# Kernel optimization log

Measured on AMD Instinct MI355X. Metric: run time of the kernel, lower is better.

The kernel has to match this reference:

```python
import jax, jax.numpy as jnp
import numpy as np

B, H, S, D = 2, 16, 2048, 64

def setup_inputs() -> dict:
    key = jax.random.key(0)
    kq, kk, kv = jax.random.split(key, 3)
    query = jax.random.normal(kq, (B, H, S, D), dtype=jnp.float32)
    key_t = jax.random.normal(kk, (B, H, S, D), dtype=jnp.float32)
    value = jax.random.normal(kv, (B, H, S, D), dtype=jnp.float32)
    return {"query": query, "key": key_t, "value": value}

def reference(query, key, value):
    d_k = query.shape[-1]
    scale = 1.0 / jnp.sqrt(jnp.asarray(d_k, dtype=query.dtype))
    # scores: [B, H, S, S]
    scores = jnp.einsum('bhqd,bhkd->bhqk', query, key) * scale
    p_attn = jax.nn.softmax(scores, axis=-1)
    output = jnp.einsum('bhqk,bhkd->bhqd', p_attn, value)
    return (output, p_attn)
```

## Files before the change

kernel.cpp:

```cpp
#include <hip/hip_runtime.h>

#define SS 2048
#define DD 64
#define QB 64
#define KVB 64
#define NT (SS / KVB)

typedef unsigned short ushort_t;
typedef __attribute__((ext_vector_type(4)))  float f32x4;
typedef __attribute__((ext_vector_type(16))) float f32x16;
typedef __attribute__((ext_vector_type(8)))  short bf16x8;
typedef __attribute__((ext_vector_type(2)))  unsigned int u32x2;

static __device__ __forceinline__ unsigned short f2bf(float f) {
    unsigned u = __builtin_bit_cast(unsigned, f);
    u += 0x7FFFu + ((u >> 16) & 1u);
    return (unsigned short)(u >> 16);
}

static __device__ __forceinline__ f32x16 zero16() {
    f32x16 z;
#pragma unroll
    for (int i = 0; i < 16; ++i) z[i] = 0.f;
    return z;
}

union PFrag { bf16x8 v; unsigned w[4]; };

#define GLL16(src, dst) \
    __builtin_amdgcn_global_load_lds((const __attribute__((address_space(1))) void*)(src), \
                                     (__attribute__((address_space(3))) void*)(dst), 16, 0, 0)

__global__ void cvt_bf16(const float* __restrict__ src, ushort_t* __restrict__ dst,
                         int n8, float scale)
{
    int i = blockIdx.x * blockDim.x + threadIdx.x;
    if (i >= n8) return;
    f32x4 a = ((const f32x4*)src)[2 * i];
    f32x4 b = ((const f32x4*)src)[2 * i + 1];
    bf16x8 o;
#pragma unroll
    for (int j = 0; j < 4; ++j) o[j] = (short)f2bf(a[j] * scale);
#pragma unroll
    for (int j = 0; j < 4; ++j) o[4 + j] = (short)f2bf(b[j] * scale);
    ((bf16x8*)dst)[i] = o;
}

__global__ void transposeV(const float* __restrict__ V, ushort_t* __restrict__ Vt)
{
    __shared__ float tile[64][65];
    const int tid = threadIdx.x;
    const int hh = blockIdx.x >> 5;
    const int kt = blockIdx.x & 31;

#pragma unroll
    for (int it = 0; it < 4; ++it) {
        int m = it * 256 + tid;
        int r = m >> 4, c4 = m & 15;
        f32x4 v = *(const f32x4*)(V + ((size_t)(hh * SS + kt * 64 + r)) * DD + c4 * 4);
#pragma unroll
        for (int j = 0; j < 4; ++j) tile[r][c4 * 4 + j] = v[j];
    }
    __syncthreads();
#pragma unroll
    for (int it = 0; it < 2; ++it) {
        int m = it * 256 + tid;
        int d = m >> 3, c8 = m & 7;
        bf16x8 o;
#pragma unroll
        for (int j = 0; j < 8; ++j) o[j] = (short)f2bf(tile[c8 * 8 + j][d]);
        *(bf16x8*)(Vt + ((size_t)hh * DD + d) * SS + kt * 64 + c8 * 8) = o;
    }
}

__global__ __launch_bounds__(256, 4)
void attn_main4(const float* __restrict__ gQ, const ushort_t* __restrict__ Kbf,
                const ushort_t* __restrict__ Vtbf, float* __restrict__ gO,
                float* __restrict__ gP)
{
    __shared__ float lsm[4][32];
    __shared__ __attribute__((aligned(16))) char shraw[33792];
    ushort_t* stage = (ushort_t*)shraw;
    float*    osm   = (float*)shraw;

    const int tid  = threadIdx.x;
    const int lane = tid & 63;
    const int wave = tid >> 6;
    const int lo5  = lane & 31;
    const int hi   = lane >> 5;
    const int qs   = wave >> 1;
    const int sub  = wave & 1;

    const int bid  = blockIdx.x;
    const int wg   = (bid & 7) * 128 + (bid >> 3);
    const int head = wg >> 5;
    const int q0b  = (wg & 31) * QB;

    const float*    Qh = gQ   + (size_t)head * SS * DD;
    const ushort_t* Kh = Kbf  + (size_t)head * SS * DD;
    const ushort_t* Vh = Vtbf + (size_t)head * DD * SS;
    float* Oh = gO + (size_t)head * SS * DD;
    float* Ph = gP + (size_t)head * SS * SS;

    const float SCALE = 0.125f * 1.44269504088896340736f;

    const int qrow = q0b + qs * 32 + lo5;
    bf16x8 qf[4];
#pragma unroll
    for (int ks = 0; ks < 4; ++ks) {
        const float* qp = Qh + (size_t)qrow * DD + ks * 16 + hi * 8;
        f32x4 a = *(const f32x4*)(qp);
        f32x4 b = *(const f32x4*)(qp + 4);
        bf16x8 o;
#pragma unroll
        for (int j = 0; j < 4; ++j) o[j] = (short)f2bf(a[j] * SCALE);
#pragma unroll
        for (int j = 0; j < 4; ++j) o[4 + j] = (short)f2bf(b[j] * SCALE);
        qf[ks] = o;
    }

    const int lgrp = lane >> 3;
    const int lchk = (lane & 7) ^ lgrp;
    const ushort_t* srcK[2]; const ushort_t* srcV[2];
#pragma unroll
    for (int j = 0; j < 2; ++j) {
        int W = wave * 2 + j;
        srcK[j] = Kh + (size_t)(W * 8 + lgrp) * DD + lchk * 8;
        srcV[j] = Vh + (size_t)(W * 8 + lgrp) * SS + lchk * 8;
    }
    const int kvl = sub * 32 + lo5;

#pragma unroll
    for (int j = 0; j < 2; ++j) GLL16(srcK[j], stage + (wave * 2 + j) * 512);
    __syncthreads();

    float ls0 = 0.f, ls1 = 0.f;
    for (int t = 0; t < NT; ++t) {
        const int buf = t & 1;
        if (t + 1 < NT) {
#pragma unroll
            for (int j = 0; j < 2; ++j)
                GLL16(srcK[j] + (size_t)(t + 1) * KVB * DD,
                      stage + (buf ^ 1) * 8192 + (wave * 2 + j) * 512);
        }
        const ushort_t* Ksb = stage + buf * 8192;
        f32x16 acc = zero16();
#pragma unroll
        for (int ks = 0; ks < 4; ++ks) {
            bf16x8 kf = *(const bf16x8*)(Ksb + kvl * 64 + ((((ks * 2) + hi) ^ (kvl & 7)) << 3));
            acc = __builtin_amdgcn_mfma_f32_32x32x16_bf16(kf, qf[ks], acc, 0, 0, 0);
        }
#pragma unroll
        for (int r = 0; r < 16; r += 2) {
            ls0 += __builtin_exp2f(acc[r]);
            ls1 += __builtin_exp2f(acc[r + 1]);
        }
        __syncthreads();
    }
    float lsum = ls0 + ls1;
    lsum += __shfl_xor(lsum, 32);
    lsm[wave][lo5] = lsum;
    __syncthreads();
    const float rinv = 1.0f / (lsm[qs * 2][lo5] + lsm[qs * 2 + 1][lo5]);

    f32x16 o0 = zero16(), o1 = zero16();
    float* prow_base = Ph + (size_t)qrow * SS;

#pragma unroll
    for (int j = 0; j < 2; ++j) {
        GLL16(srcK[j], stage + (wave * 2 + j) * 512);
        GLL16(srcV[j], stage + 4096 + (wave * 2 + j) * 512);
    }
    __syncthreads();

    for (int t = 0; t < NT; ++t) {
        const int buf = t & 1;
        if (t + 1 < NT) {
#pragma unroll
            for (int j = 0; j < 2; ++j) {
                GLL16(srcK[j] + (size_t)(t + 1) * KVB * DD,
                      stage + (buf ^ 1) * 8192 + (wave * 2 + j) * 512);
                GLL16(srcV[j] + (size_t)(t + 1) * KVB,
                      stage + (buf ^ 1) * 8192 + 4096 + (wave * 2 + j) * 512);
            }
        }
        const ushort_t* Ksb = stage + buf * 8192;
        const ushort_t* Vtb = Ksb + 4096;

        f32x16 acc = zero16();
#pragma unroll
        for (int ks = 0; ks < 4; ++ks) {
            bf16x8 kf = *(const bf16x8*)(Ksb + kvl * 64 + ((((ks * 2) + hi) ^ (kvl & 7)) << 3));
            acc = __builtin_amdgcn_mfma_f32_32x32x16_bf16(kf, qf[ks], acc, 0, 0, 0);
        }
        float pr[16];
#pragma unroll
        for (int r = 0; r < 16; ++r) pr[r] = __builtin_exp2f(acc[r]);

        float* prow = prow_base + t * KVB + sub * 32;
#pragma unroll
        for (int g = 0; g < 4; ++g) {
            f32x4 st = { pr[4*g+0] * rinv, pr[4*g+1] * rinv, pr[4*g+2] * rinv, pr[4*g+3] * rinv };
            *(f32x4*)(prow + g * 8 + hi * 4) = st;
        }

        unsigned u[8];
#pragma unroll
        for (int j = 0; j < 8; ++j)
            u[j] = (unsigned)f2bf(pr[2*j]) | ((unsigned)f2bf(pr[2*j+1]) << 16);

        unsigned s0 = __shfl_xor(u[0], 32), s1 = __shfl_xor(u[1], 32);
        unsigned s2 = __shfl_xor(u[2], 32), s3 = __shfl_xor(u[3], 32);
        unsigned s4 = __shfl_xor(u[4], 32), s5 = __shfl_xor(u[5], 32);
        unsigned s6 = __shfl_xor(u[6], 32), s7 = __shfl_xor(u[7], 32);
        PFrag pf0, pf1;
        pf0.w[0] = hi ? s2 : u[0];  pf0.w[1] = hi ? s3 : u[1];
        pf0.w[2] = hi ? u[2] : s0;  pf0.w[3] = hi ? u[3] : s1;
        pf1.w[0] = hi ? s6 : u[4];  pf1.w[1] = hi ? s7 : u[5];
        pf1.w[2] = hi ? u[6] : s4;  pf1.w[3] = hi ? u[7] : s5;

#pragma unroll
        for (int dt = 0; dt < 2; ++dt) {
            int drow = dt * 32 + lo5;
            int c0 = ((sub * 4) + 0 + hi) ^ (drow & 7);
            int c1 = ((sub * 4) + 2 + hi) ^ (drow & 7);
            bf16x8 vf0 = *(const bf16x8*)(Vtb + drow * 64 + (c0 << 3));
            bf16x8 vf1 = *(const bf16x8*)(Vtb + drow * 64 + (c1 << 3));
            f32x16& od = dt ? o1 : o0;
            od = __builtin_amdgcn_mfma_f32_32x32x16_bf16(vf0, pf0.v, od, 0, 0, 0);
            od = __builtin_amdgcn_mfma_f32_32x32x16_bf16(vf1, pf1.v, od, 0, 0, 0);
        }

        __syncthreads();
    }

#pragma unroll
    for (int dt = 0; dt < 2; ++dt) {
        const f32x16& od = dt ? o1 : o0;
#pragma unroll
        for (int g = 0; g < 4; ++g) {
#pragma unroll
            for (int j = 0; j < 4; ++j) {
                int d = dt * 32 + g * 8 + hi * 4 + j;
                osm[(wave * 64 + d) * 33 + lo5] = od[4 * g + j];
            }
        }
    }
    __syncthreads();
    {
        const int p  = tid >> 7;
        const int q  = (tid >> 2) & 31;
        const int d0 = (tid & 3) * 16;
        const float rq = 1.0f / (lsm[2 * p][q] + lsm[2 * p + 1][q]);
        float* op = Oh + (size_t)(q0b + p * 32 + q) * DD + d0;
#pragma unroll
        for (int v4 = 0; v4 < 4; ++v4) {
            f32x4 st;
#pragma unroll
            for (int j = 0; j < 4; ++j) {
                int d = d0 + v4 * 4 + j;
                st[j] = (osm[((2 * p) * 64 + d) * 33 + q] +
                         osm[((2 * p + 1) * 64 + d) * 33 + q]) * rq;
            }
            *(f32x4*)(op + v4 * 4) = st;
        }
    }
}

__global__ __launch_bounds__(256, 2)
void attn_fused(const float* __restrict__ gQ, const float* __restrict__ gK,
                const float* __restrict__ gV, float* __restrict__ gO,
                float* __restrict__ gP)
{
    __shared__ unsigned short Qs[128 * DD];
    __shared__ unsigned short Ks[64 * DD];
    __shared__ unsigned short Vt[DD * 64];

    const int tid  = threadIdx.x;
    const int lane = tid & 63;
    const int wave = tid >> 6;
    const int lo5  = lane & 31;
    const int hi   = lane >> 5;

    const int head = blockIdx.x >> 4;
    const int q0b  = (blockIdx.x & 15) * 128;

    const float* Qh = gQ + (size_t)head * SS * DD;
    const float* Kh = gK + (size_t)head * SS * DD;
    const float* Vh = gV + (size_t)head * SS * DD;
    float* Oh = gO + (size_t)head * SS * DD;
    float* Ph = gP + (size_t)head * SS * SS;

    const float SCALE = 0.125f * 1.44269504088896340736f;

#pragma unroll
    for (int it = 0; it < 8; ++it) {
        int m = it * 256 + tid;
        int q = m >> 4, d4 = m & 15;
        f32x4 v = *(const f32x4*)(Qh + (size_t)(q0b + q) * DD + d4 * 4);
        unsigned a = (unsigned)f2bf(v.x * SCALE) | ((unsigned)f2bf(v.y * SCALE) << 16);
        unsigned b = (unsigned)f2bf(v.z * SCALE) | ((unsigned)f2bf(v.w * SCALE) << 16);
        u32x2 w; w.x = a; w.y = b;
        *(u32x2*)(Qs + q * 64 + d4 * 4) = w;
    }
    __syncthreads();

    const int qrow = wave * 32 + lo5;
    bf16x8 qf[4];
#pragma unroll
    for (int ks = 0; ks < 4; ++ks)
        qf[ks] = *(const bf16x8*)(Qs + qrow * 64 + ks * 16 + hi * 8);

    auto stageK = [&](int kv0) {
#pragma unroll
        for (int it = 0; it < 4; ++it) {
            int m = it * 256 + tid;
            int kv = m >> 4, d4 = m & 15;
            f32x4 v = *(const f32x4*)(Kh + (size_t)(kv0 + kv) * DD + d4 * 4);
            unsigned a = (unsigned)f2bf(v.x) | ((unsigned)f2bf(v.y) << 16);
            unsigned b = (unsigned)f2bf(v.z) | ((unsigned)f2bf(v.w) << 16);
            int c16 = (d4 >> 1) ^ (kv & 7);
            u32x2 w; w.x = a; w.y = b;
            *(u32x2*)(Ks + kv * 64 + c16 * 8 + (d4 & 1) * 4) = w;
        }
    };
    auto stageV = [&](int kv0) {
#pragma unroll
        for (int it = 0; it < 2; ++it) {
            int m = it * 256 + tid;
            int kv2 = m >> 4, d4 = m & 15;
            const float* p0 = Vh + (size_t)(kv0 + kv2 * 2) * DD + d4 * 4;
            f32x4 v0 = *(const f32x4*)(p0);
            f32x4 v1 = *(const f32x4*)(p0 + DD);
#pragma unroll
            for (int c = 0; c < 4; ++c) {
                int d = d4 * 4 + c;
                unsigned u = (unsigned)f2bf(v0[c]) | ((unsigned)f2bf(v1[c]) << 16);
                int c16 = (kv2 >> 2) ^ (d & 7);
                *(unsigned*)(Vt + d * 64 + c16 * 8 + (kv2 & 3) * 2) = u;
            }
        }
    };

    float m_run = -1e30f, l_run = 0.f;
    for (int kv0 = 0; kv0 < SS; kv0 += 64) {
        __syncthreads();
        stageK(kv0);
        __syncthreads();
#pragma unroll
        for (int sub = 0; sub < 2; ++sub) {
            f32x16 acc = zero16();
            int kvl = sub * 32 + lo5;
#pragma unroll
            for (int ks = 0; ks < 4; ++ks) {
                bf16x8 kf = *(const bf16x8*)(Ks + kvl * 64 + ((((ks * 2) + hi) ^ (kvl & 7)) << 3));
                acc = __builtin_amdgcn_mfma_f32_32x32x16_bf16(kf, qf[ks], acc, 0, 0, 0);
            }
            float tm = acc[0];
#pragma unroll
            for (int r = 1; r < 16; ++r) tm = fmaxf(tm, acc[r]);
            float mn = fmaxf(m_run, tm);
            float sum = 0.f;
#pragma unroll
            for (int r = 0; r < 16; ++r) sum += __builtin_exp2f(acc[r] - mn);
            l_run = l_run * __builtin_exp2f(m_run - mn) + sum;
            m_run = mn;
        }
    }
    {
        float mo = __shfl_xor(m_run, 32);
        float mf = fmaxf(m_run, mo);
        float la = l_run * __builtin_exp2f(m_run - mf);
        float lb = __shfl_xor(la, 32);
        l_run = la + lb;
        m_run = mf;
    }
    const float rinv = 1.0f / l_run;

    f32x16 o0 = zero16(), o1 = zero16();
    const int qg = q0b + wave * 32 + lo5;
    float* prow_base = Ph + (size_t)qg * SS;

    for (int kv0 = 0; kv0 < SS; kv0 += 64) {
        __syncthreads();
        stageK(kv0);
        stageV(kv0);
        __syncthreads();
#pragma unroll
        for (int sub = 0; sub < 2; ++sub) {
            f32x16 acc = zero16();
            int kvl = sub * 32 + lo5;
#pragma unroll
            for (int ks = 0; ks < 4; ++ks) {
                bf16x8 kf = *(const bf16x8*)(Ks + kvl * 64 + ((((ks * 2) + hi) ^ (kvl & 7)) << 3));
                acc = __builtin_amdgcn_mfma_f32_32x32x16_bf16(kf, qf[ks], acc, 0, 0, 0);
            }
            float pr[16];
#pragma unroll
            for (int r = 0; r < 16; ++r) pr[r] = __builtin_exp2f(acc[r] - m_run);

            float* prow = prow_base + kv0 + sub * 32;
#pragma unroll
            for (int g = 0; g < 4; ++g) {
                f32x4 st = { pr[4*g+0] * rinv, pr[4*g+1] * rinv, pr[4*g+2] * rinv, pr[4*g+3] * rinv };
                *(f32x4*)(prow + g * 8 + hi * 4) = st;
            }

            unsigned u[8];
#pragma unroll
            for (int j = 0; j < 8; ++j)
                u[j] = (unsigned)f2bf(pr[2*j]) | ((unsigned)f2bf(pr[2*j+1]) << 16);

            unsigned s0 = __shfl_xor(u[0], 32), s1 = __shfl_xor(u[1], 32);
            unsigned s2 = __shfl_xor(u[2], 32), s3 = __shfl_xor(u[3], 32);
            unsigned s4 = __shfl_xor(u[4], 32), s5 = __shfl_xor(u[5], 32);
            unsigned s6 = __shfl_xor(u[6], 32), s7 = __shfl_xor(u[7], 32);
            PFrag pf0, pf1;
            pf0.w[0] = hi ? s2 : u[0];  pf0.w[1] = hi ? s3 : u[1];
            pf0.w[2] = hi ? u[2] : s0;  pf0.w[3] = hi ? u[3] : s1;
            pf1.w[0] = hi ? s6 : u[4];  pf1.w[1] = hi ? s7 : u[5];
            pf1.w[2] = hi ? u[6] : s4;  pf1.w[3] = hi ? u[7] : s5;

#pragma unroll
            for (int dt = 0; dt < 2; ++dt) {
                int drow = dt * 32 + lo5;
                int c0 = ((sub * 4) + 0 + hi) ^ (drow & 7);
                int c1 = ((sub * 4) + 2 + hi) ^ (drow & 7);
                bf16x8 vf0 = *(const bf16x8*)(Vt + drow * 64 + (c0 << 3));
                bf16x8 vf1 = *(const bf16x8*)(Vt + drow * 64 + (c1 << 3));
                f32x16& od = dt ? o1 : o0;
                od = __builtin_amdgcn_mfma_f32_32x32x16_bf16(vf0, pf0.v, od, 0, 0, 0);
                od = __builtin_amdgcn_mfma_f32_32x32x16_bf16(vf1, pf1.v, od, 0, 0, 0);
            }
        }
    }

    float* orow = Oh + (size_t)qg * DD;
#pragma unroll
    for (int dt = 0; dt < 2; ++dt) {
        const f32x16& od = dt ? o1 : o0;
#pragma unroll
        for (int g = 0; g < 4; ++g) {
            f32x4 st = { od[4*g+0] * rinv, od[4*g+1] * rinv, od[4*g+2] * rinv, od[4*g+3] * rinv };
            *(f32x4*)(orow + dt * 32 + g * 8 + hi * 4) = st;
        }
    }
}

extern "C" void kernel_launch(void* const* d_in, const int* in_sizes, int n_in,
                              void* d_out, int out_size, void* d_ws, size_t ws_size,
                              hipStream_t stream) {
    const float* Q = (const float*)d_in[0];
    const float* K = (const float*)d_in[1];
    const float* V = (const float*)d_in[2];
    float* O = (float*)d_out;
    float* P = O + (size_t)2 * 16 * SS * DD;

    const size_t HD = (size_t)32 * SS * DD;
    const size_t need = 2 * HD * sizeof(ushort_t);

    if (ws_size >= need) {
        ushort_t* Kbf  = (ushort_t*)d_ws;
        ushort_t* Vtbf = Kbf + HD;
        int n8 = (int)(HD / 8);
        hipLaunchKernelGGL(cvt_bf16, dim3(n8 / 256), dim3(256), 0, stream, K, Kbf, n8, 1.0f);
        hipLaunchKernelGGL(transposeV, dim3(1024), dim3(256), 0, stream, V, Vtbf);
        hipLaunchKernelGGL(attn_main4, dim3(1024), dim3(256), 0, stream, Q, Kbf, Vtbf, O, P);
    } else {
        hipLaunchKernelGGL(attn_fused, dim3(512), dim3(256), 0, stream, Q, K, V, O, P);
    }
}
```

Before: 212.3 us.

## Process two Q tiles per block, fusing second tile's row-sum pass into first's output pass

Each workgroup now handles 128 query rows as two 64-row halves. The row-sum pass for the second half is folded into the P/O pass of the first half, sharing the K tile loads and fragments, so the blocks make three sweeps over K/V instead of four. The K bf16 conversion and the V transpose are merged into a single prep launch to save one kernel launch. In exchange the grid is halved to 512 blocks with launch bounds of 2, and LDS and register use go up, which lowers occupancy.

```diff
diff --git a/kernel.cpp b/kernel.cpp
--- a/kernel.cpp
+++ b/kernel.cpp
@@ -2,7 +2,7 @@
 
 #define SS 2048
 #define DD 64
-#define QB 64
+#define QB 128
 #define KVB 64
 #define NT (SS / KVB)
 
@@ -31,28 +31,26 @@
     __builtin_amdgcn_global_load_lds((const __attribute__((address_space(1))) void*)(src), \
                                      (__attribute__((address_space(3))) void*)(dst), 16, 0, 0)
 
-__global__ void cvt_bf16(const float* __restrict__ src, ushort_t* __restrict__ dst,
-                         int n8, float scale)
+__global__ void prep(const float* __restrict__ K, const float* __restrict__ V,
+                     ushort_t* __restrict__ Kbf, ushort_t* __restrict__ Vt)
 {
-    int i = blockIdx.x * blockDim.x + threadIdx.x;
-    if (i >= n8) return;
-    f32x4 a = ((const f32x4*)src)[2 * i];
-    f32x4 b = ((const f32x4*)src)[2 * i + 1];
-    bf16x8 o;
-#pragma unroll
-    for (int j = 0; j < 4; ++j) o[j] = (short)f2bf(a[j] * scale);
-#pragma unroll
-    for (int j = 0; j < 4; ++j) o[4 + j] = (short)f2bf(b[j] * scale);
-    ((bf16x8*)dst)[i] = o;
-}
-
-__global__ void transposeV(const float* __restrict__ V, ushort_t* __restrict__ Vt)
-{
+    const int tid = threadIdx.x;
+    if (blockIdx.x < 2048) {
+        int i = blockIdx.x * 256 + tid;
+        f32x4 a = ((const f32x4*)K)[2 * i];
+        f32x4 b = ((const f32x4*)K)[2 * i + 1];
+        bf16x8 o;
+#pragma unroll
+        for (int j = 0; j < 4; ++j) o[j] = (short)f2bf(a[j]);
+#pragma unroll
+        for (int j = 0; j < 4; ++j) o[4 + j] = (short)f2bf(b[j]);
+        ((bf16x8*)Kbf)[i] = o;
+        return;
+    }
     __shared__ float tile[64][65];
-    const int tid = threadIdx.x;
-    const int hh = blockIdx.x >> 5;
-    const int kt = blockIdx.x & 31;
-
+    const int bid2 = blockIdx.x - 2048;
+    const int hh = bid2 >> 5;
+    const int kt = bid2 & 31;
 #pragma unroll
     for (int it = 0; it < 4; ++it) {
         int m = it * 256 + tid;
@@ -73,15 +71,14 @@
     }
 }
 
-__global__ __launch_bounds__(256, 4)
-void attn_main4(const float* __restrict__ gQ, const ushort_t* __restrict__ Kbf,
-                const ushort_t* __restrict__ Vtbf, float* __restrict__ gO,
-                float* __restrict__ gP)
+__global__ __launch_bounds__(256, 2)
+void attn_main11(const float* __restrict__ gQ, const ushort_t* __restrict__ Kbf,
+                 const ushort_t* __restrict__ Vtbf, float* __restrict__ gO,
+                 float* __restrict__ gP)
 {
-    __shared__ float lsm[4][32];
-    __shared__ __attribute__((aligned(16))) char shraw[33792];
-    ushort_t* stage = (ushort_t*)shraw;
-    float*    osm   = (float*)shraw;
+    __shared__ float lsm[2][4][32];
+    __shared__ __attribute__((aligned(16))) ushort_t stage[2][8192];
+    __shared__ float osm[4 * 64 * 33];
 
     const int tid  = threadIdx.x;
     const int lane = tid & 63;
@@ -92,9 +89,9 @@
     const int sub  = wave & 1;
 
     const int bid  = blockIdx.x;
-    const int wg   = (bid & 7) * 128 + (bid >> 3);
-    const int head = wg >> 5;
-    const int q0b  = (wg & 31) * QB;
+    const int wg   = (bid & 7) * 64 + (bid >> 3);
+    const int head = wg >> 4;
+    const int q0b  = (wg & 15) * QB;
 
     const float*    Qh = gQ   + (size_t)head * SS * DD;
     const ushort_t* Kh = Kbf  + (size_t)head * SS * DD;
@@ -104,20 +101,21 @@
 
     const float SCALE = 0.125f * 1.44269504088896340736f;
 
-    const int qrow = q0b + qs * 32 + lo5;
-    bf16x8 qf[4];
-#pragma unroll
-    for (int ks = 0; ks < 4; ++ks) {
-        const float* qp = Qh + (size_t)qrow * DD + ks * 16 + hi * 8;
-        f32x4 a = *(const f32x4*)(qp);
-        f32x4 b = *(const f32x4*)(qp + 4);
-        bf16x8 o;
-#pragma unroll
-        for (int j = 0; j < 4; ++j) o[j] = (short)f2bf(a[j] * SCALE);
-#pragma unroll
-        for (int j = 0; j < 4; ++j) o[4 + j] = (short)f2bf(b[j] * SCALE);
-        qf[ks] = o;
-    }
+    bf16x8 qfh[2][4];
+#pragma unroll
+    for (int h = 0; h < 2; ++h)
+#pragma unroll
+        for (int ks = 0; ks < 4; ++ks) {
+            const float* qp = Qh + (size_t)(q0b + h * 64 + qs * 32 + lo5) * DD + ks * 16 + hi * 8;
+            f32x4 a = *(const f32x4*)(qp);
+            f32x4 b = *(const f32x4*)(qp + 4);
+            bf16x8 o;
+#pragma unroll
+            for (int j = 0; j < 4; ++j) o[j] = (short)f2bf(a[j] * SCALE);
+#pragma unroll
+            for (int j = 0; j < 4; ++j) o[4 + j] = (short)f2bf(b[j] * SCALE);
+            qfh[h][ks] = o;
+        }
 
     const int lgrp = lane >> 3;
     const int lchk = (lane & 7) ^ lgrp;
@@ -131,7 +129,7 @@
     const int kvl = sub * 32 + lo5;
 
 #pragma unroll
-    for (int j = 0; j < 2; ++j) GLL16(srcK[j], stage + (wave * 2 + j) * 512);
+    for (int j = 0; j < 2; ++j) GLL16(srcK[j], &stage[0][(wave * 2 + j) * 512]);
     __syncthreads();
 
     float ls0 = 0.f, ls1 = 0.f;
@@ -140,15 +138,14 @@
         if (t + 1 < NT) {
 #pragma unroll
             for (int j = 0; j < 2; ++j)
-                GLL16(srcK[j] + (size_t)(t + 1) * KVB * DD,
-                      stage + (buf ^ 1) * 8192 + (wave * 2 + j) * 512);
-        }
-        const ushort_t* Ksb = stage + buf * 8192;
+                GLL16(srcK[j] + (size_t)(t + 1) * KVB * DD, &stage[buf ^ 1][(wave * 2 + j) * 512]);
+        }
+        const ushort_t* Ksb = &stage[buf][0];
         f32x16 acc = zero16();
 #pragma unroll
         for (int ks = 0; ks < 4; ++ks) {
             bf16x8 kf = *(const bf16x8*)(Ksb + kvl * 64 + ((((ks * 2) + hi) ^ (kvl & 7)) << 3));
-            acc = __builtin_amdgcn_mfma_f32_32x32x16_bf16(kf, qf[ks], acc, 0, 0, 0);
+            acc = __builtin_amdgcn_mfma_f32_32x32x16_bf16(kf, qfh[0][ks], acc, 0, 0, 0);
         }
 #pragma unroll
         for (int r = 0; r < 16; r += 2) {
@@ -157,81 +154,100 @@
         }
         __syncthreads();
     }
-    float lsum = ls0 + ls1;
-    lsum += __shfl_xor(lsum, 32);
-    lsm[wave][lo5] = lsum;
-    __syncthreads();
-    const float rinv = 1.0f / (lsm[qs * 2][lo5] + lsm[qs * 2 + 1][lo5]);
+    {
+        float l = ls0 + ls1;
+        l += __shfl_xor(l, 32);
+        lsm[0][wave][lo5] = l;
+    }
+    __syncthreads();
+    const float rinv0 = 1.0f / (lsm[0][qs * 2][lo5] + lsm[0][qs * 2 + 1][lo5]);
 
     f32x16 o0 = zero16(), o1 = zero16();
-    float* prow_base = Ph + (size_t)qrow * SS;
-
-#pragma unroll
-    for (int j = 0; j < 2; ++j) {
-        GLL16(srcK[j], stage + (wave * 2 + j) * 512);
-        GLL16(srcV[j], stage + 4096 + (wave * 2 + j) * 512);
-    }
-    __syncthreads();
-
-    for (int t = 0; t < NT; ++t) {
-        const int buf = t & 1;
-        if (t + 1 < NT) {
-#pragma unroll
-            for (int j = 0; j < 2; ++j) {
-                GLL16(srcK[j] + (size_t)(t + 1) * KVB * DD,
-                      stage + (buf ^ 1) * 8192 + (wave * 2 + j) * 512);
-                GLL16(srcV[j] + (size_t)(t + 1) * KVB,
-                      stage + (buf ^ 1) * 8192 + 4096 + (wave * 2 + j) * 512);
-            }
-        }
-        const ushort_t* Ksb = stage + buf * 8192;
-        const ushort_t* Vtb = Ksb + 4096;
-
-        f32x16 acc = zero16();
-#pragma unroll
-        for (int ks = 0; ks < 4; ++ks) {
-            bf16x8 kf = *(const bf16x8*)(Ksb + kvl * 64 + ((((ks * 2) + hi) ^ (kvl & 7)) << 3));
-            acc = __builtin_amdgcn_mfma_f32_32x32x16_bf16(kf, qf[ks], acc, 0, 0, 0);
-        }
-        float pr[16];
-#pragma unroll
-        for (int r = 0; r < 16; ++r) pr[r] = __builtin_exp2f(acc[r]);
-
-        float* prow = prow_base + t * KVB + sub * 32;
-#pragma unroll
-        for (int g = 0; g < 4; ++g) {
-            f32x4 st = { pr[4*g+0] * rinv, pr[4*g+1] * rinv, pr[4*g+2] * rinv, pr[4*g+3] * rinv };
-            *(f32x4*)(prow + g * 8 + hi * 4) = st;
-        }
-
-        unsigned u[8];
-#pragma unroll
-        for (int j = 0; j < 8; ++j)
-            u[j] = (unsigned)f2bf(pr[2*j]) | ((unsigned)f2bf(pr[2*j+1]) << 16);
-
-        unsigned s0 = __shfl_xor(u[0], 32), s1 = __shfl_xor(u[1], 32);
-        unsigned s2 = __shfl_xor(u[2], 32), s3 = __shfl_xor(u[3], 32);
-        unsigned s4 = __shfl_xor(u[4], 32), s5 = __shfl_xor(u[5], 32);
-        unsigned s6 = __shfl_xor(u[6], 32), s7 = __shfl_xor(u[7], 32);
-        PFrag pf0, pf1;
-        pf0.w[0] = hi ? s2 : u[0];  pf0.w[1] = hi ? s3 : u[1];
-        pf0.w[2] = hi ? u[2] : s0;  pf0.w[3] = hi ? u[3] : s1;
-        pf1.w[0] = hi ? s6 : u[4];  pf1.w[1] = hi ? s7 : u[5];
-        pf1.w[2] = hi ? u[6] : s4;  pf1.w[3] = hi ? u[7] : s5;
-
-#pragma unroll
-        for (int dt = 0; dt < 2; ++dt) {
-            int drow = dt * 32 + lo5;
-            int c0 = ((sub * 4) + 0 + hi) ^ (drow & 7);
-            int c1 = ((sub * 4) + 2 + hi) ^ (drow & 7);
-            bf16x8 vf0 = *(const bf16x8*)(Vtb + drow * 64 + (c0 << 3));
-            bf16x8 vf1 = *(const bf16x8*)(Vtb + drow * 64 + (c1 << 3));
-            f32x16& od = dt ? o1 : o0;
-            od = __builtin_amdgcn_mfma_f32_32x32x16_bf16(vf0, pf0.v, od, 0, 0, 0);
-            od = __builtin_amdgcn_mfma_f32_32x32x16_bf16(vf1, pf1.v, od, 0, 0, 0);
-        }
-
-        __syncthreads();
+    float lsB0 = 0.f, lsB1 = 0.f;
+    {
+        float* prow_base = Ph + (size_t)(q0b + qs * 32 + lo5) * SS;
+
+#pragma unroll
+        for (int j = 0; j < 2; ++j) {
+            GLL16(srcK[j], &stage[0][(wave * 2 + j) * 512]);
+            GLL16(srcV[j], &stage[0][4096 + (wave * 2 + j) * 512]);
+        }
+        __syncthreads();
+
+        for (int t = 0; t < NT; ++t) {
+            const int buf = t & 1;
+            if (t + 1 < NT) {
+#pragma unroll
+                for (int j = 0; j < 2; ++j) {
+                    GLL16(srcK[j] + (size_t)(t + 1) * KVB * DD, &stage[buf ^ 1][(wave * 2 + j) * 512]);
+                    GLL16(srcV[j] + (size_t)(t + 1) * KVB,      &stage[buf ^ 1][4096 + (wave * 2 + j) * 512]);
+                }
+            }
+            const ushort_t* Ksb = &stage[buf][0];
+            const ushort_t* Vtb = Ksb + 4096;
+
+            bf16x8 kf[4];
+#pragma unroll
+            for (int ks = 0; ks < 4; ++ks)
+                kf[ks] = *(const bf16x8*)(Ksb + kvl * 64 + ((((ks * 2) + hi) ^ (kvl & 7)) << 3));
+
+            f32x16 acc = zero16(), acca = zero16();
+#pragma unroll
+            for (int ks = 0; ks < 4; ++ks) {
+                acc  = __builtin_amdgcn_mfma_f32_32x32x16_bf16(kf[ks], qfh[0][ks], acc,  0, 0, 0);
+                acca = __builtin_amdgcn_mfma_f32_32x32x16_bf16(kf[ks], qfh[1][ks], acca, 0, 0, 0);
+            }
+
+#pragma unroll
+            for (int r = 0; r < 16; r += 2) {
+                lsB0 += __builtin_exp2f(acca[r]);
+                lsB1 += __builtin_exp2f(acca[r + 1]);
+            }
+
+            float pr[16];
+#pragma unroll
+            for (int r = 0; r < 16; ++r) pr[r] = __builtin_exp2f(acc[r]);
+
+            float* prow = prow_base + t * KVB + sub * 32;
+#pragma unroll
+            for (int g = 0; g < 4; ++g) {
+                f32x4 st = { pr[4*g+0] * rinv0, pr[4*g+1] * rinv0, pr[4*g+2] * rinv0, pr[4*g+3] * rinv0 };
+                *(f32x4*)(prow + g * 8 + hi * 4) = st;
+            }
+
+            unsigned u[8];
+#pragma unroll
+            for (int j = 0; j < 8; ++j)
+                u[j] = (unsigned)f2bf(pr[2*j]) | ((unsigned)f2bf(pr[2*j+1]) << 16);
+            unsigned s0 = __shfl_xor(u[0], 32), s1 = __shfl_xor(u[1], 32);
+            unsigned s2 = __shfl_xor(u[2], 32), s3 = __shfl_xor(u[3], 32);
+            unsigned s4 = __shfl_xor(u[4], 32), s5 = __shfl_xor(u[5], 32);
+            unsigned s6 = __shfl_xor(u[6], 32), s7 = __shfl_xor(u[7], 32);
+            PFrag pf0, pf1;
+            pf0.w[0] = hi ? s2 : u[0];  pf0.w[1] = hi ? s3 : u[1];
+            pf0.w[2] = hi ? u[2] : s0;  pf0.w[3] = hi ? u[3] : s1;
+            pf1.w[0] = hi ? s6 : u[4];  pf1.w[1] = hi ? s7 : u[5];
+            pf1.w[2] = hi ? u[6] : s4;  pf1.w[3] = hi ? u[7] : s5;
+
+#pragma unroll
+            for (int dt = 0; dt < 2; ++dt) {
+                int drow = dt * 32 + lo5;
+                int c0 = ((sub * 4) + 0 + hi) ^ (drow & 7);
+                int c1 = ((sub * 4) + 2 + hi) ^ (drow & 7);
+                bf16x8 vf0 = *(const bf16x8*)(Vtb + drow * 64 + (c0 << 3));
+                bf16x8 vf1 = *(const bf16x8*)(Vtb + drow * 64 + (c1 << 3));
+                f32x16& od = dt ? o1 : o0;
+                od = __builtin_amdgcn_mfma_f32_32x32x16_bf16(vf0, pf0.v, od, 0, 0, 0);
+                od = __builtin_amdgcn_mfma_f32_32x32x16_bf16(vf1, pf1.v, od, 0, 0, 0);
+            }
+
+            __syncthreads();
+        }
+    }
+    {
+        float l = lsB0 + lsB1;
+        l += __shfl_xor(l, 32);
+        lsm[1][wave][lo5] = l;
     }
 
 #pragma unroll
@@ -251,8 +267,112 @@
         const int p  = tid >> 7;
         const int q  = (tid >> 2) & 31;
         const int d0 = (tid & 3) * 16;
-        const float rq = 1.0f / (lsm[2 * p][q] + lsm[2 * p + 1][q]);
+        const float rq = 1.0f / (lsm[0][2 * p][q] + lsm[0][2 * p + 1][q]);
         float* op = Oh + (size_t)(q0b + p * 32 + q) * DD + d0;
+#pragma unroll
+        for (int v4 = 0; v4 < 4; ++v4) {
+            f32x4 st;
+#pragma unroll
+            for (int j = 0; j < 4; ++j) {
+                int d = d0 + v4 * 4 + j;
+                st[j] = (osm[((2 * p) * 64 + d) * 33 + q] +
+                         osm[((2 * p + 1) * 64 + d) * 33 + q]) * rq;
+            }
+            *(f32x4*)(op + v4 * 4) = st;
+        }
+    }
+    __syncthreads();
+    const float rinv1 = 1.0f / (lsm[1][qs * 2][lo5] + lsm[1][qs * 2 + 1][lo5]);
+
+    o0 = zero16(); o1 = zero16();
+    {
+        float* prow_base = Ph + (size_t)(q0b + 64 + qs * 32 + lo5) * SS;
+
+#pragma unroll
+        for (int j = 0; j < 2; ++j) {
+            GLL16(srcK[j], &stage[0][(wave * 2 + j) * 512]);
+            GLL16(srcV[j], &stage[0][4096 + (wave * 2 + j) * 512]);
+        }
+        __syncthreads();
+
+        for (int t = 0; t < NT; ++t) {
+            const int buf = t & 1;
+            if (t + 1 < NT) {
+#pragma unroll
+                for (int j = 0; j < 2; ++j) {
+                    GLL16(srcK[j] + (size_t)(t + 1) * KVB * DD, &stage[buf ^ 1][(wave * 2 + j) * 512]);
+                    GLL16(srcV[j] + (size_t)(t + 1) * KVB,      &stage[buf ^ 1][4096 + (wave * 2 + j) * 512]);
+                }
+            }
+            const ushort_t* Ksb = &stage[buf][0];
+            const ushort_t* Vtb = Ksb + 4096;
+
+            f32x16 acc = zero16();
+#pragma unroll
+            for (int ks = 0; ks < 4; ++ks) {
+                bf16x8 kf = *(const bf16x8*)(Ksb + kvl * 64 + ((((ks * 2) + hi) ^ (kvl & 7)) << 3));
+                acc = __builtin_amdgcn_mfma_f32_32x32x16_bf16(kf, qfh[1][ks], acc, 0, 0, 0);
+            }
+            float pr[16];
+#pragma unroll
+            for (int r = 0; r < 16; ++r) pr[r] = __builtin_exp2f(acc[r]);
+
+            float* prow = prow_base + t * KVB + sub * 32;
+#pragma unroll
+            for (int g = 0; g < 4; ++g) {
+                f32x4 st = { pr[4*g+0] * rinv1, pr[4*g+1] * rinv1, pr[4*g+2] * rinv1, pr[4*g+3] * rinv1 };
+                *(f32x4*)(prow + g * 8 + hi * 4) = st;
+            }
+
+            unsigned u[8];
+#pragma unroll
+            for (int j = 0; j < 8; ++j)
+                u[j] = (unsigned)f2bf(pr[2*j]) | ((unsigned)f2bf(pr[2*j+1]) << 16);
+            unsigned s0 = __shfl_xor(u[0], 32), s1 = __shfl_xor(u[1], 32);
+            unsigned s2 = __shfl_xor(u[2], 32), s3 = __shfl_xor(u[3], 32);
+            unsigned s4 = __shfl_xor(u[4], 32), s5 = __shfl_xor(u[5], 32);
+            unsigned s6 = __shfl_xor(u[6], 32), s7 = __shfl_xor(u[7], 32);
+            PFrag pf0, pf1;
+            pf0.w[0] = hi ? s2 : u[0];  pf0.w[1] = hi ? s3 : u[1];
+            pf0.w[2] = hi ? u[2] : s0;  pf0.w[3] = hi ? u[3] : s1;
+            pf1.w[0] = hi ? s6 : u[4];  pf1.w[1] = hi ? s7 : u[5];
+            pf1.w[2] = hi ? u[6] : s4;  pf1.w[3] = hi ? u[7] : s5;
+
+#pragma unroll
+            for (int dt = 0; dt < 2; ++dt) {
+                int drow = dt * 32 + lo5;
+                int c0 = ((sub * 4) + 0 + hi) ^ (drow & 7);
+                int c1 = ((sub * 4) + 2 + hi) ^ (drow & 7);
+                bf16x8 vf0 = *(const bf16x8*)(Vtb + drow * 64 + (c0 << 3));
+                bf16x8 vf1 = *(const bf16x8*)(Vtb + drow * 64 + (c1 << 3));
+                f32x16& od = dt ? o1 : o0;
+                od = __builtin_amdgcn_mfma_f32_32x32x16_bf16(vf0, pf0.v, od, 0, 0, 0);
+                od = __builtin_amdgcn_mfma_f32_32x32x16_bf16(vf1, pf1.v, od, 0, 0, 0);
+            }
+
+            __syncthreads();
+        }
+    }
+
+#pragma unroll
+    for (int dt = 0; dt < 2; ++dt) {
+        const f32x16& od = dt ? o1 : o0;
+#pragma unroll
+        for (int g = 0; g < 4; ++g) {
+#pragma unroll
+            for (int j = 0; j < 4; ++j) {
+                int d = dt * 32 + g * 8 + hi * 4 + j;
+                osm[(wave * 64 + d) * 33 + lo5] = od[4 * g + j];
+            }
+        }
+    }
+    __syncthreads();
+    {
+        const int p  = tid >> 7;
+        const int q  = (tid >> 2) & 31;
+        const int d0 = (tid & 3) * 16;
+        const float rq = 1.0f / (lsm[1][2 * p][q] + lsm[1][2 * p + 1][q]);
+        float* op = Oh + (size_t)(q0b + 64 + p * 32 + q) * DD + d0;
 #pragma unroll
         for (int v4 = 0; v4 < 4; ++v4) {
             f32x4 st;
@@ -462,10 +582,8 @@
     if (ws_size >= need) {
         ushort_t* Kbf  = (ushort_t*)d_ws;
         ushort_t* Vtbf = Kbf + HD;
-        int n8 = (int)(HD / 8);
-        hipLaunchKernelGGL(cvt_bf16, dim3(n8 / 256), dim3(256), 0, stream, K, Kbf, n8, 1.0f);
-        hipLaunchKernelGGL(transposeV, dim3(1024), dim3(256), 0, stream, V, Vtbf);
-        hipLaunchKernelGGL(attn_main4, dim3(1024), dim3(256), 0, stream, Q, Kbf, Vtbf, O, P);
+        hipLaunchKernelGGL(prep, dim3(3072), dim3(256), 0, stream, K, V, Kbf, Vtbf);
+        hipLaunchKernelGGL(attn_main11, dim3(512), dim3(256), 0, stream, Q, Kbf, Vtbf, O, P);
     } else {
         hipLaunchKernelGGL(attn_fused, dim3(512), dim3(256), 0, stream, Q, K, V, O, P);
     }
```

After: 234.1 us. 10.3% more time.
